# Performance work log

Measured on AMD Instinct MI355X. Metric: run time of the kernel, lower is better.

Reference implementation:

```python
import jax, jax.numpy as jnp
import numpy as np

BATCH, NODES, CH_IN, CH_OUT, N_EXPERTS = 8, 8192, 128, 128, 64

def setup_inputs() -> dict:
    key = jax.random.key(0)
    kx, kw, ks = jax.random.split(key, 3)
    x = jax.random.normal(kx, (BATCH, NODES, CH_IN), dtype=jnp.float32)
    # std = fan_in**-0.5 per self_init
    W = jax.random.normal(kw, (N_EXPERTS, CH_OUT, CH_IN), dtype=jnp.float32) * (CH_IN ** -0.5)
    sel = jax.random.randint(ks, (NODES,), 0, N_EXPERTS, dtype=jnp.int64)
    return {"x": x, "sel": sel, "W": W}

def reference(x, sel, W):
    # x: (b, n, j), W[sel]: (n, i, j) -> out: (b, n, i)
    Wsel = W[sel]  # gather a (ch_out, ch_in) matrix per node
    return jnp.einsum('bnj,nij->bni', x, Wsel)
```

## Files before the change

kernel.cpp:

```cpp
#include <hip/hip_runtime.h>

#define BATCH   8
#define NODES   8192
#define CH      128
#define NEXP    64
#define TN      16
#define MAXP    (NODES + NEXP * TN)
#define NTILES  (MAXP / TN)
#define NSORT   64
#define SLICE   (NODES / NSORT)

typedef __attribute__((ext_vector_type(8))) short bf16x8;
typedef __attribute__((ext_vector_type(4))) float f32x4;

__device__ __forceinline__ bf16x8 cvt8(f32x4 lo, f32x4 hi) {
    bf16x8 r;
    #pragma unroll
    for (int i = 0; i < 4; ++i) {
        r[i]     = (short)__builtin_bit_cast(unsigned short, static_cast<__bf16>(lo[i]));
        r[i + 4] = (short)__builtin_bit_cast(unsigned short, static_cast<__bf16>(hi[i]));
    }
    return r;
}

__global__ __launch_bounds__(256)
void prep1_kernel(const int* __restrict__ sel, const float* __restrict__ W,
                  short* __restrict__ Wbf, int* __restrict__ sorted,
                  int* __restrict__ gcnt)
{
    const int t   = threadIdx.x;
    const int blk = blockIdx.x;

    {
        const size_t base = (size_t)blk * (CH * CH / 4);
        const float* ws = W   + base;
        short*       wd = Wbf + base;
        #pragma unroll
        for (int i = 0; i < 2; ++i) {
            int idx = (i * 256 + t) * 8;
            f32x4 lo = *reinterpret_cast<const f32x4*>(ws + idx);
            f32x4 hi = *reinterpret_cast<const f32x4*>(ws + idx + 4);
            *reinterpret_cast<bf16x8*>(wd + idx) = cvt8(lo, hi);
        }
    }

    {
        const int si = blk * 256 + t;
        if (si < MAXP) sorted[si] = -1;
    }

    if (blk < NSORT) {
        __shared__ int hist[NEXP];
        if (t < NEXP) hist[t] = 0;
        __syncthreads();
        if (t < SLICE) atomicAdd(&hist[sel[blk * SLICE + t]], 1);
        __syncthreads();
        if (t < NEXP) gcnt[blk * NEXP + t] = hist[t];
    }
}

__global__ __launch_bounds__(256)
void prep2_kernel(const int* __restrict__ sel, const int* __restrict__ gcnt,
                  int* __restrict__ sorted)
{
    const int t   = threadIdx.x;
    const int blk = blockIdx.x;

    __shared__ int cursor[NEXP];

    if (t < NEXP) {
        int cnt = 0, own = 0;
        for (int s = 0; s < NSORT; ++s) {
            int g = gcnt[s * NEXP + t];
            own += (s < blk) ? g : 0;
            cnt += g;
        }
        int p = (cnt + TN - 1) & ~(TN - 1);
        int scan = p;
        #pragma unroll
        for (int d = 1; d < NEXP; d <<= 1) {
            int v = __shfl_up(scan, d);
            if (t >= d) scan += v;
        }
        cursor[t] = (scan - p) + own;
    }
    __syncthreads();

    if (t < SLICE) {
        int n = blk * SLICE + t;
        int e = sel[n];
        int pos = atomicAdd(&cursor[e], 1);
        sorted[pos] = n;
    }
}

__global__ __launch_bounds__(256)
void gemm_kernel(const float* __restrict__ x, const int* __restrict__ sel,
                 const short* __restrict__ Wbf, float* __restrict__ out,
                 const int* __restrict__ sorted)
{
    __shared__ int s_nodes[TN];
    __shared__ int s_expert;

    const int tid  = threadIdx.x;
    const int tile = blockIdx.x;

    if (tid < TN) s_nodes[tid] = sorted[tile * TN + tid];
    if (tid == 0) {
        int n0 = sorted[tile * TN];
        s_expert = (n0 >= 0) ? sel[n0] : -1;
    }
    __syncthreads();

    const int e = s_expert;
    if (e < 0) return;

    const int wave = tid >> 6;
    const int lane = tid & 63;
    const int m16  = lane & 15;
    const int quad = lane >> 4;

    int          nodej[2];
    const float* xrow[2];
    #pragma unroll
    for (int jt = 0; jt < 2; ++jt) {
        int j    = wave * 32 + jt * 16 + m16;
        int node = s_nodes[j >> 3];
        int b    = j & 7;
        nodej[jt] = node;
        int nd   = (node >= 0) ? node : 0;
        xrow[jt] = x + ((size_t)(b * NODES + nd)) * CH;
    }
    const short* wbase = Wbf + (size_t)e * CH * CH;

    f32x4 acc[2][8];
    #pragma unroll
    for (int jt = 0; jt < 2; ++jt)
        #pragma unroll
        for (int ct = 0; ct < 8; ++ct)
            acc[jt][ct] = (f32x4){0.f, 0.f, 0.f, 0.f};

    #pragma unroll
    for (int kk = 0; kk < 4; ++kk) {
        const int k0 = kk * 32 + quad * 8;

        bf16x8 xfrag[2];
        #pragma unroll
        for (int jt = 0; jt < 2; ++jt) {
            const float* p = xrow[jt] + k0;
            f32x4 lo = *reinterpret_cast<const f32x4*>(p);
            f32x4 hi = *reinterpret_cast<const f32x4*>(p + 4);
            xfrag[jt] = cvt8(lo, hi);
        }

        #pragma unroll
        for (int ct = 0; ct < 8; ++ct) {
            bf16x8 wfrag = *reinterpret_cast<const bf16x8*>(
                wbase + (size_t)(ct * 16 + m16) * CH + k0);
            acc[0][ct] = __builtin_amdgcn_mfma_f32_16x16x32_bf16(
                             wfrag, xfrag[0], acc[0][ct], 0, 0, 0);
            acc[1][ct] = __builtin_amdgcn_mfma_f32_16x16x32_bf16(
                             wfrag, xfrag[1], acc[1][ct], 0, 0, 0);
        }
    }

    #pragma unroll
    for (int jt = 0; jt < 2; ++jt) {
        int node = nodej[jt];
        if (node < 0) continue;
        int j = wave * 32 + jt * 16 + m16;
        int b = j & 7;
        float* orow = out + ((size_t)(b * NODES + node)) * CH;
        #pragma unroll
        for (int ct = 0; ct < 8; ++ct)
            *reinterpret_cast<f32x4*>(orow + ct * 16 + quad * 4) = acc[jt][ct];
    }
}

extern "C" void kernel_launch(void* const* d_in, const int* in_sizes, int n_in,
                              void* d_out, int out_size, void* d_ws, size_t ws_size,
                              hipStream_t stream)
{
    const float* x   = (const float*)d_in[0];
    const int*   sel = (const int*)  d_in[1];
    const float* W   = (const float*)d_in[2];
    float*       out = (float*)d_out;

    short* Wbf    = (short*)d_ws;
    int*   sorted = (int*)((char*)d_ws + (size_t)NEXP * CH * CH * sizeof(short));
    int*   gcnt   = sorted + MAXP;

    prep1_kernel<<<256, 256, 0, stream>>>(sel, W, Wbf, sorted, gcnt);
    prep2_kernel<<<NSORT, 256, 0, stream>>>(sel, gcnt, sorted);
    gemm_kernel<<<NTILES, 256, 0, stream>>>(x, sel, Wbf, out, sorted);
}
```

Baseline: 110.4 us.

## Stage expert weights in swizzled LDS via async global_load_lds and prefetch x

The prep kernel now writes bf16 weights in an XOR-swizzled layout. The GEMM block copies the full 128x128 expert matrix into shared memory with global_load_lds, while all x rows are loaded into registers up front. MFMA weight fragments are then read from LDS with the swizzle, which avoids bank conflicts. This replaces the repeated per-wave global reads of W and overlaps the x loads with the W copy. In exchange it uses 32KB of LDS per block, which may lower occupancy, and adds register pressure from the prefetched x values.

```diff
diff --git a/kernel.cpp b/kernel.cpp
--- a/kernel.cpp
+++ b/kernel.cpp
@@ -13,6 +13,9 @@
 typedef __attribute__((ext_vector_type(8))) short bf16x8;
 typedef __attribute__((ext_vector_type(4))) float f32x4;
 
+typedef const __attribute__((address_space(1))) unsigned int gu32;
+typedef __attribute__((address_space(3))) unsigned int lu32;
+
 __device__ __forceinline__ bf16x8 cvt8(f32x4 lo, f32x4 hi) {
     bf16x8 r;
     #pragma unroll
@@ -31,17 +34,17 @@
     const int t   = threadIdx.x;
     const int blk = blockIdx.x;
 
-    {
-        const size_t base = (size_t)blk * (CH * CH / 4);
-        const float* ws = W   + base;
-        short*       wd = Wbf + base;
-        #pragma unroll
-        for (int i = 0; i < 2; ++i) {
-            int idx = (i * 256 + t) * 8;
-            f32x4 lo = *reinterpret_cast<const f32x4*>(ws + idx);
-            f32x4 hi = *reinterpret_cast<const f32x4*>(ws + idx + 4);
-            *reinterpret_cast<bf16x8*>(wd + idx) = cvt8(lo, hi);
-        }
+    #pragma unroll
+    for (int i = 0; i < 2; ++i) {
+        const int g8  = blk * 512 + i * 256 + t;
+        const int e   = g8 >> 11;
+        const int row = (g8 & 2047) >> 4;
+        const int chk = g8 & 15;
+        const float* ws = W + (size_t)g8 * 8;
+        f32x4 lo = *reinterpret_cast<const f32x4*>(ws);
+        f32x4 hi = *reinterpret_cast<const f32x4*>(ws + 4);
+        short* wd = Wbf + ((size_t)e << 14) + row * CH + ((chk ^ (row & 7)) << 3);
+        *reinterpret_cast<bf16x8*>(wd) = cvt8(lo, hi);
     }
 
     {
@@ -99,6 +102,7 @@
                  const short* __restrict__ Wbf, float* __restrict__ out,
                  const int* __restrict__ sorted)
 {
+    __shared__ short s_w[CH * CH];
     __shared__ int s_nodes[TN];
     __shared__ int s_expert;
 
@@ -131,7 +135,37 @@
         int nd   = (node >= 0) ? node : 0;
         xrow[jt] = x + ((size_t)(b * NODES + nd)) * CH;
     }
-    const short* wbase = Wbf + (size_t)e * CH * CH;
+
+    f32x4 xl[2][4][2];
+    #pragma unroll
+    for (int jt = 0; jt < 2; ++jt)
+        #pragma unroll
+        for (int kk = 0; kk < 4; ++kk) {
+            const float* p = xrow[jt] + kk * 32 + quad * 8;
+            xl[jt][kk][0] = *reinterpret_cast<const f32x4*>(p);
+            xl[jt][kk][1] = *reinterpret_cast<const f32x4*>(p + 4);
+        }
+
+    {
+        const char* gsrc = (const char*)(Wbf + ((size_t)e << 14))
+                         + wave * 8192 + lane * 16;
+        char* ldst = (char*)s_w + wave * 8192;
+        #pragma unroll
+        for (int i = 0; i < 8; ++i) {
+            __builtin_amdgcn_global_load_lds(
+                (gu32*)(gsrc + i * 1024),
+                (lu32*)(ldst + i * 1024),
+                16, 0, 0);
+        }
+    }
+    __syncthreads();
+
+    bf16x8 xfrag[2][4];
+    #pragma unroll
+    for (int jt = 0; jt < 2; ++jt)
+        #pragma unroll
+        for (int kk = 0; kk < 4; ++kk)
+            xfrag[jt][kk] = cvt8(xl[jt][kk][0], xl[jt][kk][1]);
 
     f32x4 acc[2][8];
     #pragma unroll
@@ -142,25 +176,15 @@
 
     #pragma unroll
     for (int kk = 0; kk < 4; ++kk) {
-        const int k0 = kk * 32 + quad * 8;
-
-        bf16x8 xfrag[2];
-        #pragma unroll
-        for (int jt = 0; jt < 2; ++jt) {
-            const float* p = xrow[jt] + k0;
-            f32x4 lo = *reinterpret_cast<const f32x4*>(p);
-            f32x4 hi = *reinterpret_cast<const f32x4*>(p + 4);
-            xfrag[jt] = cvt8(lo, hi);
-        }
-
         #pragma unroll
         for (int ct = 0; ct < 8; ++ct) {
-            bf16x8 wfrag = *reinterpret_cast<const bf16x8*>(
-                wbase + (size_t)(ct * 16 + m16) * CH + k0);
+            const int row = ct * 16 + m16;
+            const bf16x8 wfrag = *reinterpret_cast<const bf16x8*>(
+                s_w + row * CH + (((kk * 4 + quad) ^ (row & 7)) << 3));
             acc[0][ct] = __builtin_amdgcn_mfma_f32_16x16x32_bf16(
-                             wfrag, xfrag[0], acc[0][ct], 0, 0, 0);
+                             wfrag, xfrag[0][kk], acc[0][ct], 0, 0, 0);
             acc[1][ct] = __builtin_amdgcn_mfma_f32_16x16x32_bf16(
-                             wfrag, xfrag[1], acc[1][ct], 0, 0, 0);
+                             wfrag, xfrag[1][kk], acc[1][ct], 0, 0, 0);
         }
     }
 
```

New measurement: 102.2 us. 1.08x faster.
